# Performance work log

Hardware: AMD Instinct MI355X
Metric: run time of the kernel (lower is better)

## Reference

```python
import jax, jax.numpy as jnp
import numpy as np

D_MODEL = 1024
FEED = 4096
HEADS = 16
EPS = 1e-5


def _ln(x, g, b):
    mu = jnp.mean(x, axis=-1, keepdims=True)
    var = jnp.var(x, axis=-1, keepdims=True)
    return (x - mu) * jax.lax.rsqrt(var + EPS) * g + b


def setup_inputs() -> dict:
    key = jax.random.key(0)
    ks = jax.random.split(key, 8)
    s = 0.02
    return {
        "src": jax.random.normal(ks[0], (8, 512, D_MODEL), jnp.float32),
        "wq": jax.random.normal(ks[1], (D_MODEL, D_MODEL), jnp.float32) * s,
        "bq": jnp.zeros((D_MODEL,), jnp.float32),
        "wk": jax.random.normal(ks[2], (D_MODEL, D_MODEL), jnp.float32) * s,
        "bk": jnp.zeros((D_MODEL,), jnp.float32),
        "wv": jax.random.normal(ks[3], (D_MODEL, D_MODEL), jnp.float32) * s,
        "bv": jnp.zeros((D_MODEL,), jnp.float32),
        "g1": jnp.ones((D_MODEL,), jnp.float32),
        "be1": jnp.zeros((D_MODEL,), jnp.float32),
        "w1": jax.random.normal(ks[4], (D_MODEL, FEED), jnp.float32) * s,
        "b1": jnp.zeros((FEED,), jnp.float32),
        "w2": jax.random.normal(ks[5], (FEED, D_MODEL), jnp.float32) * s,
        "b2": jnp.zeros((D_MODEL,), jnp.float32),
        "g2": jnp.ones((D_MODEL,), jnp.float32),
        "be2": jnp.zeros((D_MODEL,), jnp.float32),
    }


def reference(src, wq, bq, wk, bk, wv, bv, g1, be1, w1, b1, w2, b2, g2, be2):
    bs, seq, d = src.shape
    dk = d // HEADS
    q = src @ wq + bq
    k = src @ wk + bk
    v = src @ wv + bv
    # [B, H, S, dk]
    q = q.reshape(bs, seq, HEADS, dk).transpose(0, 2, 1, 3)
    k = k.reshape(bs, seq, HEADS, dk).transpose(0, 2, 1, 3)
    v = v.reshape(bs, seq, HEADS, dk).transpose(0, 2, 1, 3)
    scores = jnp.einsum('bhqd,bhkd->bhqk', q, k)  # no mask (src_mask unused in original)
    att = jax.nn.softmax(scores / jnp.sqrt(jnp.float32(dk)), axis=-1)
    ctx = jnp.einsum('bhqk,bhkd->bhqd', att, v)
    ctx = ctx.transpose(0, 2, 1, 3).reshape(bs, seq, d)  # concat heads
    x = _ln(ctx + src, g1, be1)
    # FFN (dropout = identity at eval)
    h = jax.nn.relu(x @ w1 + b1)
    y = h @ w2 + b2
    return _ln(y + x, g2, be2)
```

## Files before the change

### kernel.cpp

```cpp
#include <hip/hip_runtime.h>
#include <hip/hip_bf16.h>
#include <stdint.h>

#define DM   1024
#define FF   4096
#define NH   16
#define DK   64
#define SEQ  512
#define NTOK 4096

typedef __attribute__((ext_vector_type(8))) unsigned short ushort8;
typedef __attribute__((ext_vector_type(4))) unsigned short ushort4v;
typedef __attribute__((ext_vector_type(8))) short bf16x8;
typedef __attribute__((ext_vector_type(4))) float f32x4;

__device__ __forceinline__ float bf2f(unsigned short u) {
  union { unsigned int i; float f; } v; v.i = ((unsigned int)u) << 16; return v.f;
}
__device__ __forceinline__ unsigned short f2bf(float f) {
  union { float fl; unsigned int i; } v; v.fl = f;
  v.i += 0x7fffu + ((v.i >> 16) & 1u);
  return (unsigned short)(v.i >> 16);
}

__device__ __forceinline__ void gload16(const unsigned short* g, unsigned short* l) {
  __builtin_amdgcn_global_load_lds(
      (const __attribute__((address_space(1))) unsigned int*)g,
      (__attribute__((address_space(3))) unsigned int*)l, 16, 0, 0);
}

__global__ __launch_bounds__(256)
void f32_to_bf16(const float* __restrict__ in, unsigned short* __restrict__ out,
                 long n) {
  long i = ((long)blockIdx.x * 256 + threadIdx.x) * 4;
  if (i + 3 < n) {
    f32x4 v = *(const f32x4*)(in + i);
    ushort4v o;
#pragma unroll
    for (int j = 0; j < 4; j++) o[j] = f2bf(v[j]);
    *(ushort4v*)(out + i) = o;
  }
}

__global__ void transpose_f2b(const float* __restrict__ in, int ldin,
                              unsigned short* __restrict__ out, int ldout) {
  __shared__ unsigned short tile[32][33];
  const int tx = threadIdx.x, ty = threadIdx.y;
  const long r0 = (long)blockIdx.y * 32, c0 = (long)blockIdx.x * 32;
#pragma unroll
  for (int i = 0; i < 4; i++)
    tile[ty + i * 8][tx] = f2bf(in[(r0 + ty + i * 8) * ldin + c0 + tx]);
  __syncthreads();
#pragma unroll
  for (int i = 0; i < 4; i++)
    out[(c0 + ty + i * 8) * ldout + r0 + tx] = tile[tx][ty + i * 8];
}

__global__ void transpose_v(const unsigned short* __restrict__ QKV,
                            unsigned short* __restrict__ Vt) {
  __shared__ unsigned short tile[32][33];
  const int tx = threadIdx.x, ty = threadIdx.y;
  const int bh = blockIdx.z, b = bh >> 4, h = bh & 15;
  const int s0 = blockIdx.y * 32, d0 = blockIdx.x * 32;
  const unsigned short* inb = QKV + (long)(b * SEQ) * 3072 + 2048 + h * 64;
#pragma unroll
  for (int i = 0; i < 4; i++)
    tile[ty + i * 8][tx] = inb[(long)(s0 + ty + i * 8) * 3072 + d0 + tx];
  __syncthreads();
#pragma unroll
  for (int i = 0; i < 4; i++)
    Vt[(long)bh * (DK * SEQ) + (long)(d0 + ty + i * 8) * SEQ + s0 + tx] =
        tile[tx][ty + i * 8];
}

__global__ void concat3(const float* __restrict__ a, const float* __restrict__ b,
                        const float* __restrict__ c, float* __restrict__ o) {
  int i = blockIdx.x * 256 + threadIdx.x;
  if (i < 3072)
    o[i] = (i < 1024) ? a[i] : ((i < 2048) ? b[i - 1024] : c[i - 2048]);
}

#define WAITBAR4 asm volatile("s_waitcnt vmcnt(4)\ns_barrier" ::: "memory")
#define WAITBAR0 asm volatile("s_waitcnt vmcnt(0)\ns_barrier" ::: "memory")

template <bool RELU, bool PARTIAL>
__global__ __launch_bounds__(512, 2)
void gemm256(const unsigned short* __restrict__ A, int lda,
             const unsigned short* __restrict__ B, int ldb,
             const float* __restrict__ bias,
             unsigned short* __restrict__ C,
             unsigned short* __restrict__ P1,
             unsigned short* __restrict__ P2,
             unsigned short* __restrict__ P3,
             int ldc, int nTN) {
  __shared__ unsigned short sm[49152];
  const int tid = threadIdx.x;
  const int lane = tid & 63;
  const int wid = tid >> 6;
  const int wr = wid >> 2, wc = wid & 3;

  const unsigned int T = gridDim.x;
  const unsigned int q8 = T >> 3;
  const unsigned int x = blockIdx.x;
  const unsigned int swz = (x & 7) * q8 + (x >> 3);
  const long bm = (long)(swz / nTN) * 256;
  const long bn = (long)(swz % nTN) * 256;
  const long kbase = (long)blockIdx.y * 1024;

  f32x4 acc[8][4];
#pragma unroll
  for (int mf = 0; mf < 8; mf++)
#pragma unroll
    for (int nf = 0; nf < 4; nf++) acc[mf][nf] = f32x4{0.f, 0.f, 0.f, 0.f};

  const int strow = tid >> 2;
  const int scol = (((tid & 3) ^ ((strow >> 1) & 3)) << 3);
  const unsigned short* pA0 = A + (bm + strow) * lda + kbase + scol;
  const unsigned short* pA1 = A + (bm + 128 + strow) * lda + kbase + scol;
  const unsigned short* pB0 = B + (bn + strow) * ldb + kbase + scol;
  const unsigned short* pB1 = B + (bn + 128 + strow) * ldb + kbase + scol;
  unsigned short* ldst = sm + tid * 8;

  int offA[8], offB[4];
#pragma unroll
  for (int mf = 0; mf < 8; mf++) {
    const int ra = wr * 128 + mf * 16 + (lane & 15);
    offA[mf] = ra * 32 + ((((lane >> 4) ^ ((ra >> 1) & 3))) << 3);
  }
#pragma unroll
  for (int nf = 0; nf < 4; nf++) {
    const int rb = wc * 64 + nf * 16 + (lane & 15);
    offB[nf] = rb * 32 + ((((lane >> 4) ^ ((rb >> 1) & 3))) << 3);
  }

#define GSTEP(tt, SB) do {                                   \
    gload16(pA0 + (tt) * 32, ldst + (SB) * 8192);            \
    gload16(pA1 + (tt) * 32, ldst + (SB) * 8192 + 4096);     \
    gload16(pB0 + (tt) * 32, ldst + 24576 + (SB) * 8192);    \
    gload16(pB1 + (tt) * 32, ldst + 24576 + (SB) * 8192 + 4096); \
  } while (0)

#define CSTEP(BB) do {                                                        \
    bf16x8 a_[8], b_[4];                                                      \
    _Pragma("unroll")                                                         \
    for (int mf = 0; mf < 8; mf++)                                            \
      a_[mf] = *(const bf16x8*)(sm + (BB) * 8192 + offA[mf]);                 \
    _Pragma("unroll")                                                         \
    for (int nf = 0; nf < 4; nf++)                                            \
      b_[nf] = *(const bf16x8*)(sm + 24576 + (BB) * 8192 + offB[nf]);         \
    __builtin_amdgcn_s_setprio(1);                                            \
    _Pragma("unroll")                                                         \
    for (int mf = 0; mf < 8; mf++)                                            \
      _Pragma("unroll")                                                       \
      for (int nf = 0; nf < 4; nf++)                                          \
        acc[mf][nf] = __builtin_amdgcn_mfma_f32_16x16x32_bf16(                \
            a_[mf], b_[nf], acc[mf][nf], 0, 0, 0);                            \
    __builtin_amdgcn_s_setprio(0);                                            \
  } while (0)

  GSTEP(0, 0);
  GSTEP(1, 1);
  WAITBAR4;
  for (int t = 0; t < 30; t += 3) {
    GSTEP(t + 2, 2); CSTEP(0); WAITBAR4;
    GSTEP(t + 3, 0); CSTEP(1); WAITBAR4;
    GSTEP(t + 4, 1); CSTEP(2); WAITBAR4;
  }
  CSTEP(0); WAITBAR0;
  CSTEP(1);
#undef GSTEP
#undef CSTEP

  unsigned short* Cw = C;
  if (PARTIAL) {
    const int kc = blockIdx.y;
    Cw = (kc == 0) ? C : (kc == 1) ? P1 : (kc == 2) ? P2 : P3;
  }
  const long r0 = bm + wr * 128 + ((lane >> 4) << 2);
  const int c0 = (int)bn + wc * 64 + (lane & 15);
#pragma unroll
  for (int nf = 0; nf < 4; nf++) {
    const int col = c0 + nf * 16;
    const float bv = PARTIAL ? 0.f : bias[col];
#pragma unroll
    for (int mf = 0; mf < 8; mf++) {
#pragma unroll
      for (int i = 0; i < 4; i++) {
        float v = acc[mf][nf][i] + bv;
        if (RELU) v = fmaxf(v, 0.f);
        Cw[(r0 + mf * 16 + i) * ldc + col] = f2bf(v);
      }
    }
  }
}

__global__ __launch_bounds__(512)
void attn_kernel(const unsigned short* __restrict__ QKV,
                 const unsigned short* __restrict__ Vt,
                 unsigned short* __restrict__ CTX) {
  const int qt = blockIdx.x;
  const int bh = blockIdx.y;
  const int b = bh >> 4, h = bh & 15;
  const int tid = threadIdx.x;
  const int lane = tid & 63;
  const int wid = tid >> 6;

  __shared__ unsigned short Ks[64][72];
  __shared__ unsigned short Vs[64][72];
  __shared__ unsigned short Ps[8][16][72];

  const int qrow0 = qt * 128 + wid * 16;
  const unsigned short* Qb = QKV + (long)(b * SEQ + qrow0) * 3072 + h * 64;
  bf16x8 aq[2];
#pragma unroll
  for (int ks = 0; ks < 2; ks++)
    aq[ks] = *(const bf16x8*)(Qb + (long)(lane & 15) * 3072 + ks * 32 +
                              (lane >> 4) * 8);

  f32x4 acc_o[4];
#pragma unroll
  for (int n = 0; n < 4; n++) acc_o[n] = f32x4{0.f, 0.f, 0.f, 0.f};
  float rsum[4] = {0.f, 0.f, 0.f, 0.f};

  const int sr = tid >> 3;
  const int sc = (tid & 7) * 8;
  const unsigned short* Kg = QKV + (long)(b * SEQ) * 3072 + 1024 + h * 64 + sc;
  const unsigned short* Vg = Vt + (long)bh * (DK * SEQ) + (long)sr * SEQ + sc;

  ushort8 kr = *(const ushort8*)(Kg + (long)sr * 3072);
  ushort8 vr = *(const ushort8*)(Vg);

#pragma unroll
  for (int c = 0; c < 8; ++c) {
    __syncthreads();
    *(ushort8*)(&Ks[sr][sc]) = kr;
    *(ushort8*)(&Vs[sr][sc]) = vr;
    if (c < 7) {
      kr = *(const ushort8*)(Kg + (long)((c + 1) * 64 + sr) * 3072);
      vr = *(const ushort8*)(Vg + (c + 1) * 64);
    }
    __syncthreads();

    f32x4 s[4];
#pragma unroll
    for (int n = 0; n < 4; n++) s[n] = f32x4{0.f, 0.f, 0.f, 0.f};
#pragma unroll
    for (int ks = 0; ks < 2; ks++) {
      bf16x8 kf[4];
#pragma unroll
      for (int n = 0; n < 4; n++)
        kf[n] = *(const bf16x8*)(&Ks[n * 16 + (lane & 15)][ks * 32 + (lane >> 4) * 8]);
#pragma unroll
      for (int n = 0; n < 4; n++)
        s[n] = __builtin_amdgcn_mfma_f32_16x16x32_bf16(aq[ks], kf[n], s[n], 0, 0, 0);
    }

#pragma unroll
    for (int n = 0; n < 4; n++) {
#pragma unroll
      for (int i = 0; i < 4; i++) {
        const float p = __expf(s[n][i] * 0.125f);
        rsum[i] += p;
        Ps[wid][(lane >> 4) * 4 + i][n * 16 + (lane & 15)] = f2bf(p);
      }
    }

#pragma unroll
    for (int ks = 0; ks < 2; ks++) {
      bf16x8 pa = *(const bf16x8*)(&Ps[wid][lane & 15][ks * 32 + (lane >> 4) * 8]);
      bf16x8 vf[4];
#pragma unroll
      for (int n = 0; n < 4; n++)
        vf[n] = *(const bf16x8*)(&Vs[n * 16 + (lane & 15)][ks * 32 + (lane >> 4) * 8]);
#pragma unroll
      for (int n = 0; n < 4; n++)
        acc_o[n] = __builtin_amdgcn_mfma_f32_16x16x32_bf16(pa, vf[n], acc_o[n], 0, 0, 0);
    }
  }

#pragma unroll
  for (int i = 0; i < 4; i++) {
#pragma unroll
    for (int off = 1; off < 16; off <<= 1) rsum[i] += __shfl_xor(rsum[i], off, 64);
  }

  const long orow0 = (long)(b * SEQ + qrow0);
#pragma unroll
  for (int i = 0; i < 4; i++) {
    const float inv = 1.f / rsum[i];
    const long r = orow0 + (lane >> 4) * 4 + i;
#pragma unroll
    for (int n = 0; n < 4; n++)
      CTX[r * DM + h * 64 + n * 16 + (lane & 15)] = f2bf(acc_o[n][i] * inv);
  }
}

__global__ __launch_bounds__(256)
void ln1_kernel(const unsigned short* __restrict__ X,
                const float* __restrict__ R,
                const float* __restrict__ g,
                const float* __restrict__ be,
                float* __restrict__ Of,
                unsigned short* __restrict__ Ob) {
  const int t = blockIdx.x;
  const int tid = threadIdx.x;
  const long base = (long)t * DM + tid * 4;
  __shared__ float red[8];

  ushort4v xv = *(const ushort4v*)(X + base);
  f32x4 rv = *(const f32x4*)(R + base);
  float v[4];
#pragma unroll
  for (int j = 0; j < 4; j++) v[j] = bf2f(xv[j]) + rv[j];
  float s = v[0] + v[1] + v[2] + v[3];
  float q = v[0] * v[0] + v[1] * v[1] + v[2] * v[2] + v[3] * v[3];
#pragma unroll
  for (int off = 1; off < 64; off <<= 1) {
    s += __shfl_xor(s, off, 64);
    q += __shfl_xor(q, off, 64);
  }
  if ((tid & 63) == 0) { red[tid >> 6] = s; red[4 + (tid >> 6)] = q; }
  __syncthreads();
  s = red[0] + red[1] + red[2] + red[3];
  q = red[4] + red[5] + red[6] + red[7];
  const float mu = s * (1.f / DM);
  const float var = q * (1.f / DM) - mu * mu;
  const float rstd = rsqrtf(fmaxf(var, 0.f) + 1e-5f);

  f32x4 gv = *(const f32x4*)(g + tid * 4);
  f32x4 bv = *(const f32x4*)(be + tid * 4);
  f32x4 of;
  ushort4v ob;
#pragma unroll
  for (int j = 0; j < 4; j++) {
    of[j] = (v[j] - mu) * rstd * gv[j] + bv[j];
    ob[j] = f2bf(of[j]);
  }
  *(f32x4*)(Of + base) = of;
  *(ushort4v*)(Ob + base) = ob;
}

__global__ __launch_bounds__(256)
void ln2_kernel(const unsigned short* __restrict__ P0,
                const unsigned short* __restrict__ P1,
                const unsigned short* __restrict__ P2,
                const unsigned short* __restrict__ P3,
                const float* __restrict__ b2,
                const float* __restrict__ R,
                const float* __restrict__ g,
                const float* __restrict__ be,
                float* __restrict__ O) {
  const int t = blockIdx.x;
  const int tid = threadIdx.x;
  const long base = (long)t * DM + tid * 4;
  __shared__ float red[8];

  ushort4v p0 = *(const ushort4v*)(P0 + base);
  ushort4v p1 = *(const ushort4v*)(P1 + base);
  ushort4v p2 = *(const ushort4v*)(P2 + base);
  ushort4v p3 = *(const ushort4v*)(P3 + base);
  f32x4 bb = *(const f32x4*)(b2 + tid * 4);
  f32x4 rv = *(const f32x4*)(R + base);
  float v[4];
#pragma unroll
  for (int j = 0; j < 4; j++)
    v[j] = bf2f(p0[j]) + bf2f(p1[j]) + bf2f(p2[j]) + bf2f(p3[j]) + bb[j] + rv[j];
  float s = v[0] + v[1] + v[2] + v[3];
  float q = v[0] * v[0] + v[1] * v[1] + v[2] * v[2] + v[3] * v[3];
#pragma unroll
  for (int off = 1; off < 64; off <<= 1) {
    s += __shfl_xor(s, off, 64);
    q += __shfl_xor(q, off, 64);
  }
  if ((tid & 63) == 0) { red[tid >> 6] = s; red[4 + (tid >> 6)] = q; }
  __syncthreads();
  s = red[0] + red[1] + red[2] + red[3];
  q = red[4] + red[5] + red[6] + red[7];
  const float mu = s * (1.f / DM);
  const float var = q * (1.f / DM) - mu * mu;
  const float rstd = rsqrtf(fmaxf(var, 0.f) + 1e-5f);

  f32x4 gv = *(const f32x4*)(g + tid * 4);
  f32x4 bv = *(const f32x4*)(be + tid * 4);
  f32x4 of;
#pragma unroll
  for (int j = 0; j < 4; j++) of[j] = (v[j] - mu) * rstd * gv[j] + bv[j];
  *(f32x4*)(O + base) = of;
}

extern "C" void kernel_launch(void* const* d_in, const int* in_sizes, int n_in,
                              void* d_out, int out_size, void* d_ws, size_t ws_size,
                              hipStream_t stream) {
  const float* src = (const float*)d_in[0];
  const float* wq  = (const float*)d_in[1];
  const float* bq  = (const float*)d_in[2];
  const float* wk  = (const float*)d_in[3];
  const float* bk  = (const float*)d_in[4];
  const float* wv  = (const float*)d_in[5];
  const float* bv  = (const float*)d_in[6];
  const float* g1  = (const float*)d_in[7];
  const float* be1 = (const float*)d_in[8];
  const float* w1  = (const float*)d_in[9];
  const float* b1  = (const float*)d_in[10];
  const float* w2  = (const float*)d_in[11];
  const float* b2  = (const float*)d_in[12];
  const float* g2  = (const float*)d_in[13];
  const float* be2 = (const float*)d_in[14];
  float* out = (float*)d_out;

  char* ws = (char*)d_ws;
  const size_t MB = 1024 * 1024;
  unsigned short* srcb  = (unsigned short*)(ws + 0);
  unsigned short* WqkvT = (unsigned short*)(ws + 8 * MB);
  float*          bqkv  = (float*)(ws + 14 * MB);
  unsigned short* W1T   = (unsigned short*)(ws + 15 * MB);
  unsigned short* W2T   = (unsigned short*)(ws + 23 * MB);
  unsigned short* QKV   = (unsigned short*)(ws + 31 * MB);
  unsigned short* Vtb   = (unsigned short*)(ws + 55 * MB);
  unsigned short* CTX   = (unsigned short*)(ws + 63 * MB);
  unsigned short* X1    = (unsigned short*)(ws + 71 * MB);
  float*          X1f   = (float*)(ws + 79 * MB);
  unsigned short* Hb    = (unsigned short*)(ws + 31 * MB);
  unsigned short* Pk0   = (unsigned short*)(ws + 0);
  unsigned short* Pk1   = (unsigned short*)(ws + 15 * MB);
  unsigned short* Pk2   = (unsigned short*)(ws + 63 * MB);
  unsigned short* Pk3   = (unsigned short*)(ws + 71 * MB);
  if (ws_size < 95 * MB) return;

  const dim3 t32(32, 8, 1);
  f32_to_bf16<<<4096, 256, 0, stream>>>(src, srcb, (long)NTOK * DM);
  transpose_f2b<<<dim3(32, 32), t32, 0, stream>>>(wq, 1024, WqkvT, 1024);
  transpose_f2b<<<dim3(32, 32), t32, 0, stream>>>(wk, 1024, WqkvT + 1024 * 1024, 1024);
  transpose_f2b<<<dim3(32, 32), t32, 0, stream>>>(wv, 1024, WqkvT + 2 * 1024 * 1024, 1024);
  transpose_f2b<<<dim3(128, 32), t32, 0, stream>>>(w1, 4096, W1T, 1024);
  transpose_f2b<<<dim3(32, 128), t32, 0, stream>>>(w2, 1024, W2T, 4096);
  concat3<<<12, 256, 0, stream>>>(bq, bk, bv, bqkv);

  gemm256<false, false><<<dim3(192, 1), 512, 0, stream>>>(
      srcb, 1024, WqkvT, 1024, bqkv, QKV, nullptr, nullptr, nullptr, 3072, 12);
  transpose_v<<<dim3(2, 16, 128), t32, 0, stream>>>(QKV, Vtb);
  attn_kernel<<<dim3(4, 128), 512, 0, stream>>>(QKV, Vtb, CTX);
  ln1_kernel<<<NTOK, 256, 0, stream>>>(CTX, src, g1, be1, X1f, X1);
  gemm256<true, false><<<dim3(256, 1), 512, 0, stream>>>(
      X1, 1024, W1T, 1024, b1, Hb, nullptr, nullptr, nullptr, 4096, 16);
  gemm256<false, true><<<dim3(64, 4), 512, 0, stream>>>(
      Hb, 4096, W2T, 4096, nullptr, Pk0, Pk1, Pk2, Pk3, 1024, 4);
  ln2_kernel<<<NTOK, 256, 0, stream>>>(Pk0, Pk1, Pk2, Pk3, b2, X1f, g2, be2, out);
}
```

Before: 193.3 us.

## Restructure GEMM mainloop to double-buffered BK=64 with interleaved half-tile loads

The 256x256 bf16 GEMM main loop now uses two LDS buffers of 64-wide K tiles instead of three 32-wide buffers, raising shared memory from 96KB to 128KB. Each iteration splits the next tile's global loads into four quarter-groups and interleaves them with four 4x4 MFMA blocks, separated by barriers. The aim is to hide load latency and cut the number of barriers per K step. In exchange it uses more LDS and a more fragile wait/barrier schedule. The last iteration also prefetches one tile past the K range, which wastes bandwidth and may read out of bounds.

```diff
diff --git a/kernel.cpp b/kernel.cpp
--- a/kernel.cpp
+++ b/kernel.cpp
@@ -79,9 +79,6 @@
   if (i < 3072)
     o[i] = (i < 1024) ? a[i] : ((i < 2048) ? b[i - 1024] : c[i - 2048]);
 }
-
-#define WAITBAR4 asm volatile("s_waitcnt vmcnt(4)\ns_barrier" ::: "memory")
-#define WAITBAR0 asm volatile("s_waitcnt vmcnt(0)\ns_barrier" ::: "memory")
 
 template <bool RELU, bool PARTIAL>
 __global__ __launch_bounds__(512, 2)
@@ -93,7 +90,7 @@
              unsigned short* __restrict__ P2,
              unsigned short* __restrict__ P3,
              int ldc, int nTN) {
-  __shared__ unsigned short sm[49152];
+  __shared__ unsigned short sm[65536];
   const int tid = threadIdx.x;
   const int lane = tid & 63;
   const int wid = tid >> 6;
@@ -114,62 +111,79 @@
     for (int nf = 0; nf < 4; nf++) acc[mf][nf] = f32x4{0.f, 0.f, 0.f, 0.f};
 
   const int strow = tid >> 2;
-  const int scol = (((tid & 3) ^ ((strow >> 1) & 3)) << 3);
-  const unsigned short* pA0 = A + (bm + strow) * lda + kbase + scol;
-  const unsigned short* pA1 = A + (bm + 128 + strow) * lda + kbase + scol;
-  const unsigned short* pB0 = B + (bn + strow) * ldb + kbase + scol;
-  const unsigned short* pB1 = B + (bn + 128 + strow) * ldb + kbase + scol;
-  unsigned short* ldst = sm + tid * 8;
-
+  const int scol = (((tid & 3) ^ ((tid >> 3) & 3)) << 3);
+  const unsigned short* pA = A + (bm + strow) * lda + kbase + scol;
+  const unsigned short* pB = B + (bn + strow) * ldb + kbase + scol;
+  unsigned short* dA = sm + tid * 8;
+  unsigned short* dB = sm + 32768 + tid * 8;
+
+  const int g = lane >> 4;
   int offA[8], offB[4];
 #pragma unroll
   for (int mf = 0; mf < 8; mf++) {
-    const int ra = wr * 128 + mf * 16 + (lane & 15);
-    offA[mf] = ra * 32 + ((((lane >> 4) ^ ((ra >> 1) & 3))) << 3);
+    const int rm = wr * 128 + mf * 16 + (lane & 15);
+    offA[mf] = rm * 32 + ((g ^ ((rm >> 1) & 3)) << 3);
   }
 #pragma unroll
   for (int nf = 0; nf < 4; nf++) {
     const int rb = wc * 64 + nf * 16 + (lane & 15);
-    offB[nf] = rb * 32 + ((((lane >> 4) ^ ((rb >> 1) & 3))) << 3);
-  }
-
-#define GSTEP(tt, SB) do {                                   \
-    gload16(pA0 + (tt) * 32, ldst + (SB) * 8192);            \
-    gload16(pA1 + (tt) * 32, ldst + (SB) * 8192 + 4096);     \
-    gload16(pB0 + (tt) * 32, ldst + 24576 + (SB) * 8192);    \
-    gload16(pB1 + (tt) * 32, ldst + 24576 + (SB) * 8192 + 4096); \
-  } while (0)
-
-#define CSTEP(BB) do {                                                        \
-    bf16x8 a_[8], b_[4];                                                      \
-    _Pragma("unroll")                                                         \
-    for (int mf = 0; mf < 8; mf++)                                            \
-      a_[mf] = *(const bf16x8*)(sm + (BB) * 8192 + offA[mf]);                 \
-    _Pragma("unroll")                                                         \
-    for (int nf = 0; nf < 4; nf++)                                            \
-      b_[nf] = *(const bf16x8*)(sm + 24576 + (BB) * 8192 + offB[nf]);         \
+    offB[nf] = rb * 32 + ((g ^ ((rb >> 1) & 3)) << 3);
+  }
+
+#define GA(kt, ks, rh, bu) gload16(pA + (long)(rh) * 128 * lda + (kt) * 64 + (ks) * 32, \
+                                   dA + (bu) * 16384 + (ks) * 8192 + (rh) * 4096)
+#define GB(kt, ks, rh, bu) gload16(pB + (long)(rh) * 128 * ldb + (kt) * 64 + (ks) * 32, \
+                                   dB + (bu) * 16384 + (ks) * 8192 + (rh) * 4096)
+#define MF16(AR, BR, MO)                                                      \
+  do {                                                                        \
     __builtin_amdgcn_s_setprio(1);                                            \
     _Pragma("unroll")                                                         \
-    for (int mf = 0; mf < 8; mf++)                                            \
+    for (int mf = 0; mf < 4; mf++)                                            \
       _Pragma("unroll")                                                       \
       for (int nf = 0; nf < 4; nf++)                                          \
-        acc[mf][nf] = __builtin_amdgcn_mfma_f32_16x16x32_bf16(                \
-            a_[mf], b_[nf], acc[mf][nf], 0, 0, 0);                            \
+        acc[(MO) + mf][nf] = __builtin_amdgcn_mfma_f32_16x16x32_bf16(         \
+            AR[mf], BR[nf], acc[(MO) + mf][nf], 0, 0, 0);                     \
     __builtin_amdgcn_s_setprio(0);                                            \
   } while (0)
 
-  GSTEP(0, 0);
-  GSTEP(1, 1);
-  WAITBAR4;
-  for (int t = 0; t < 30; t += 3) {
-    GSTEP(t + 2, 2); CSTEP(0); WAITBAR4;
-    GSTEP(t + 3, 0); CSTEP(1); WAITBAR4;
-    GSTEP(t + 4, 1); CSTEP(2); WAITBAR4;
-  }
-  CSTEP(0); WAITBAR0;
-  CSTEP(1);
-#undef GSTEP
-#undef CSTEP
+  GA(0, 0, 0, 0); GA(0, 0, 1, 0); GA(0, 1, 0, 0); GA(0, 1, 1, 0);
+  GB(0, 0, 0, 0); GB(0, 0, 1, 0); GB(0, 1, 0, 0); GB(0, 1, 1, 0);
+
+  for (int t = 0; t < 16; ++t) {
+    const int c = t & 1, n2 = c ^ 1;
+    const int k1 = t + 1;
+    const unsigned short* smAc = sm + c * 16384;
+    const unsigned short* smBc = sm + 32768 + c * 16384;
+    bf16x8 a0[4], a1[4], a2[4], a3[4], b0[4], b1[4];
+
+    GA(k1, 0, 0, n2); GA(k1, 0, 1, n2);
+    asm volatile("s_waitcnt vmcnt(2)\ns_barrier" ::: "memory");
+#pragma unroll
+    for (int mf = 0; mf < 4; mf++) a0[mf] = *(const bf16x8*)(smAc + offA[mf]);
+#pragma unroll
+    for (int nf = 0; nf < 4; nf++) b0[nf] = *(const bf16x8*)(smBc + offB[nf]);
+    MF16(a0, b0, 0);
+    GA(k1, 1, 0, n2); GA(k1, 1, 1, n2);
+#pragma unroll
+    for (int mf = 0; mf < 4; mf++) a1[mf] = *(const bf16x8*)(smAc + offA[4 + mf]);
+    asm volatile("s_barrier" ::: "memory");
+    MF16(a1, b0, 4);
+    GB(k1, 0, 0, n2); GB(k1, 0, 1, n2);
+#pragma unroll
+    for (int mf = 0; mf < 4; mf++) a2[mf] = *(const bf16x8*)(smAc + 8192 + offA[mf]);
+#pragma unroll
+    for (int nf = 0; nf < 4; nf++) b1[nf] = *(const bf16x8*)(smBc + 8192 + offB[nf]);
+    asm volatile("s_barrier" ::: "memory");
+    MF16(a2, b1, 0);
+    GB(k1, 1, 0, n2); GB(k1, 1, 1, n2);
+#pragma unroll
+    for (int mf = 0; mf < 4; mf++) a3[mf] = *(const bf16x8*)(smAc + 8192 + offA[4 + mf]);
+    asm volatile("s_waitcnt lgkmcnt(0)\ns_barrier" ::: "memory");
+    MF16(a3, b1, 4);
+  }
+#undef GA
+#undef GB
+#undef MF16
 
   unsigned short* Cw = C;
   if (PARTIAL) {
```

Result: no change. 189.7 us (-1.8%).
